# Optimization experiments

Measured on AMD Instinct MI355X. Metric: run time of the kernel, lower is better.

Reference implementation:

```python
import jax, jax.numpy as jnp
import numpy as np

# Dimensions (see shape_source): B batch, N atoms, M neighbors
B, N, M = 32, 2048, 12
F_IN, F_OUT = 64, 25          # atom_in_fea_num, atom_out_fea_num (25 fixed by Linear(25,1))
GROUPS = ((0, 683), (683, 1366), (1366, 2048))  # contiguous atom-type partition of N
EPS = 1e-5                    # BatchNorm1d eps


def setup_inputs() -> dict:
    key = jax.random.key(0)
    ks = jax.random.split(key, 9)
    atom = jax.random.normal(ks[0], (B, N, F_IN), jnp.float32)
    bond = jax.random.normal(ks[1], (B, N, M), jnp.float32)
    adj_matrix = jax.random.randint(ks[2], (B, N, M), 0, N)  # neighbor indices into N
    s_in = 1.0 / np.sqrt(F_IN)
    s_out = 1.0 / np.sqrt(F_OUT)
    # per-atom-type linear layers, stacked [G, F_IN, F_OUT]
    type_w = jax.random.uniform(ks[3], (len(GROUPS), F_IN, F_OUT), jnp.float32, -s_in, s_in)
    type_b = jax.random.uniform(ks[4], (len(GROUPS), F_OUT), jnp.float32, -s_in, s_in)
    gamma = jnp.ones((F_OUT,), jnp.float32)   # BatchNorm weight
    beta = jnp.zeros((F_OUT,), jnp.float32)   # BatchNorm bias
    conv_w = jax.random.uniform(ks[5], (F_OUT, F_OUT), jnp.float32, -s_out, s_out)
    conv_b = jax.random.uniform(ks[6], (F_OUT,), jnp.float32, -s_out, s_out)
    out_w = jax.random.uniform(ks[7], (F_OUT, 1), jnp.float32, -s_out, s_out)
    out_b = jax.random.uniform(ks[8], (1,), jnp.float32, -s_out, s_out)
    return dict(atom=atom, bond=bond, adj_matrix=adj_matrix, type_w=type_w,
                type_b=type_b, gamma=gamma, beta=beta, conv_w=conv_w,
                conv_b=conv_b, out_w=out_w, out_b=out_b)


def reference(atom, bond, adj_matrix, type_w, type_b, gamma, beta, conv_w, conv_b, out_w, out_b):
    # 1) per-atom-type grouped linear (+relu, AtomTypeLayer), scatter-assembled -> [B,N,F_OUT]
    parts = [jax.nn.relu(jnp.einsum('bnf,fo->bno', atom[:, s:e], type_w[g]) + type_b[g])
             for g, (s, e) in enumerate(GROUPS)]
    h = jnp.concatenate(parts, axis=1)
    # 2) BatchNorm1d over channels F_OUT, batch stats over (B, N); Dropout is identity in eval
    mean = h.mean(axis=(0, 1))
    var = h.var(axis=(0, 1))
    h = (h - mean) * jax.lax.rsqrt(var + EPS) * gamma + beta
    # 3) AtomConvLayer: gather neighbor features via adj_matrix, weight by bond, reduce, linear, relu
    nbr = jax.vmap(lambda hb, ab: hb[ab])(h, adj_matrix)         # [B,N,M,F_OUT]
    msg = jnp.einsum('bnm,bnmf->bnf', bond, nbr)                  # [B,N,F_OUT]
    a = jax.nn.relu(msg @ conv_w + conv_b)
    # 4) mean-pool over atoms, final linear, relu, squeeze
    e = a.mean(axis=1) @ out_w + out_b                            # [B,1]
    return jax.nn.relu(e)[..., 0]                                 # [B]
```

## Files before the change

### kernel.cpp

```cpp
#include <hip/hip_runtime.h>
#include <hip/hip_bf16.h>

#define Bn 32
#define Nn 2048
#define Mn 12
#define FIN 64
#define FOUT 25
#define HROW 32
#define EPSBN 1e-5f

#define K1_BLOCKS 1056
#define NPART K1_BLOCKS
#define K3_BLOCKS 1024
#define NROWS 65536

__global__ __launch_bounds__(256) void k1_typelinear(
    const float* __restrict__ atom,
    const float* __restrict__ type_w,
    const float* __restrict__ type_b,
    float* __restrict__ h,
    float* __restrict__ psum,
    float* __restrict__ psq)
{
    const int blk = blockIdx.x;
    const int b = blk / 33;
    const int rem = blk % 33;
    const int g = rem / 11;
    const int chunk = rem % 11;
    const int s0 = g * 683;
    const int e0 = (g == 2) ? 2048 : (g + 1) * 683;
    const int tid = threadIdx.x;
    const int a = tid & 63;
    const int q = __builtin_amdgcn_readfirstlane(tid >> 6);
    const int n = s0 + chunk * 64 + a;
    const bool act = (n < e0);

    float acc[FOUT];
    #pragma unroll
    for (int o = 0; o < FOUT; ++o) acc[o] = 0.0f;

    if (act) {
        float av[16];
        const float4* ap = reinterpret_cast<const float4*>(
            atom + ((size_t)b * Nn + n) * FIN + q * 16);
        #pragma unroll
        for (int i = 0; i < 4; ++i) {
            float4 v = ap[i];
            av[4 * i + 0] = v.x; av[4 * i + 1] = v.y;
            av[4 * i + 2] = v.z; av[4 * i + 3] = v.w;
        }
        const float* wg = type_w + (size_t)g * (FIN * FOUT) + q * 16 * FOUT;
        #pragma unroll
        for (int f = 0; f < 16; ++f) {
            const float x = av[f];
            #pragma unroll
            for (int o = 0; o < FOUT; ++o)
                acc[o] = fmaf(x, wg[f * FOUT + o], acc[o]);
        }
    }

    __shared__ float sm[3][64][26];
    if (q > 0) {
        #pragma unroll
        for (int o = 0; o < FOUT; ++o) sm[q - 1][a][o] = acc[o];
    }
    __syncthreads();
    if (q != 0) return;

    #pragma unroll
    for (int o = 0; o < FOUT; ++o)
        acc[o] += (sm[0][a][o] + sm[1][a][o]) + sm[2][a][o];

    if (act) {
        const float* bg = type_b + (size_t)g * FOUT;
        #pragma unroll
        for (int o = 0; o < FOUT; ++o)
            acc[o] = fmaxf(acc[o] + bg[o], 0.0f);
        float* hp = h + ((size_t)b * Nn + n) * HROW;
        float4* hp4 = reinterpret_cast<float4*>(hp);
        #pragma unroll
        for (int i = 0; i < 6; ++i) {
            float4 v;
            v.x = acc[4 * i + 0]; v.y = acc[4 * i + 1];
            v.z = acc[4 * i + 2]; v.w = acc[4 * i + 3];
            hp4[i] = v;
        }
        {
            float4 v; v.x = acc[24]; v.y = 0.0f; v.z = 0.0f; v.w = 0.0f;
            hp4[6] = v;
        }
    } else {
        #pragma unroll
        for (int o = 0; o < FOUT; ++o) acc[o] = 0.0f;
    }

    float bs[FOUT], bq[FOUT];
    #pragma unroll
    for (int o = 0; o < FOUT; ++o) {
        float s = acc[o];
        float qq = acc[o] * acc[o];
        #pragma unroll
        for (int m = 1; m < 64; m <<= 1) {
            s  += __shfl_xor(s,  m, 64);
            qq += __shfl_xor(qq, m, 64);
        }
        bs[o] = s; bq[o] = qq;
    }
    if (a == 0) {
        #pragma unroll
        for (int o = 0; o < FOUT; ++o)
            psum[(size_t)o * NPART + blk] = bs[o];
    } else if (a == 1) {
        #pragma unroll
        for (int o = 0; o < FOUT; ++o)
            psq[(size_t)o * NPART + blk] = bq[o];
    }
}

__global__ __launch_bounds__(256) void k2_bnstats(
    const float* __restrict__ psum,
    const float* __restrict__ psq,
    const float* __restrict__ gamma,
    const float* __restrict__ beta,
    float* __restrict__ AC)
{
    const int c = blockIdx.x;
    const int tid = threadIdx.x;
    const int lane = tid & 63;
    const int w = tid >> 6;
    const float4* ps4 = reinterpret_cast<const float4*>(psum + (size_t)c * NPART);
    const float4* pq4 = reinterpret_cast<const float4*>(psq  + (size_t)c * NPART);
    float4 v = ps4[tid];
    float4 qv = pq4[tid];
    float s1 = (v.x + v.y) + (v.z + v.w);
    float s2 = (qv.x + qv.y) + (qv.z + qv.w);
    if (tid < (NPART / 4 - 256)) {
        float4 v2 = ps4[tid + 256];
        float4 q2 = pq4[tid + 256];
        s1 += (v2.x + v2.y) + (v2.z + v2.w);
        s2 += (q2.x + q2.y) + (q2.z + q2.w);
    }
    #pragma unroll
    for (int m = 1; m < 64; m <<= 1) {
        s1 += __shfl_xor(s1, m, 64);
        s2 += __shfl_xor(s2, m, 64);
    }
    __shared__ float r1[4], r2[4];
    if (lane == 0) { r1[w] = s1; r2[w] = s2; }
    __syncthreads();
    if (tid == 0) {
        const float S1 = (r1[0] + r1[1]) + (r1[2] + r1[3]);
        const float S2 = (r2[0] + r2[1]) + (r2[2] + r2[3]);
        const float inv_cnt = 1.0f / (float)NROWS;
        const float mean = S1 * inv_cnt;
        const float var = S2 * inv_cnt - mean * mean;
        const float aa = gamma[c] * rsqrtf(var + EPSBN);
        AC[c] = aa;
        AC[28 + c] = beta[c] - mean * aa;
    }
}

__global__ __launch_bounds__(256) void k3_conv(
    const float* __restrict__ h,
    const float* __restrict__ bond,
    const int*   __restrict__ adj,
    const float* __restrict__ AC,
    const float* __restrict__ conv_w,
    const float* __restrict__ conv_b,
    const float* __restrict__ out_w,
    float* __restrict__ pe)
{
    const int blk = blockIdx.x;
    const int b = blk & 31;
    const int chunk = blk >> 5;
    const int tid = threadIdx.x;
    const int w = tid >> 6;
    const int lane = tid & 63;
    const int g = lane >> 3;
    const int c = lane & 7;

    __shared__ __align__(16) float wT[FOUT][28];
    __shared__ __align__(16) float msgn_s[4][16][36];

    for (int t = tid; t < FOUT * 28; t += 256) {
        const int o = t / 28, f = t - o * 28;
        float wv = 0.0f;
        if (f < FOUT)      wv = conv_w[f * FOUT + o];
        else if (f == 25)  wv = conv_b[o];
        else if (f == 26)  wv = out_w[o];
        wT[o][f] = wv;
    }

    const float* hb = h + (size_t)b * (Nn * HROW);
    const int atom0 = chunk * 64 + w * 16;

    const float4 Ai = *reinterpret_cast<const float4*>(AC + 4 * c);
    const float4 Ci = *reinterpret_cast<const float4*>(AC + 28 + 4 * c);

    __syncthreads();

    #pragma unroll
    for (int p = 0; p < 2; ++p) {
        const int an = atom0 + p * 8 + g;
        const size_t arow = (size_t)b * Nn + an;
        const int4*   ajp = reinterpret_cast<const int4*>(adj + arow * Mn);
        const float4* bpp = reinterpret_cast<const float4*>(bond + arow * Mn);
        const int4 A0 = ajp[0], A1 = ajp[1], A2 = ajp[2];
        const float4 B0 = bpp[0], B1 = bpp[1], B2 = bpp[2];
        const int ai[12] = {A0.x, A0.y, A0.z, A0.w,
                            A1.x, A1.y, A1.z, A1.w,
                            A2.x, A2.y, A2.z, A2.w};
        const float bw[12] = {B0.x, B0.y, B0.z, B0.w,
                              B1.x, B1.y, B1.z, B1.w,
                              B2.x, B2.y, B2.z, B2.w};
        float4 macc = {0.0f, 0.0f, 0.0f, 0.0f};
        float bsum = 0.0f;
        #pragma unroll
        for (int j = 0; j < 12; ++j) {
            const float wj = bw[j];
            bsum += wj;
            const float4 hv = *reinterpret_cast<const float4*>(
                hb + (size_t)ai[j] * HROW + c * 4);
            macc.x = fmaf(wj, hv.x, macc.x);
            macc.y = fmaf(wj, hv.y, macc.y);
            macc.z = fmaf(wj, hv.z, macc.z);
            macc.w = fmaf(wj, hv.w, macc.w);
        }
        if (c < 7) {
            float4 mn;
            mn.x = fmaf(Ai.x, macc.x, Ci.x * bsum);
            mn.y = fmaf(Ai.y, macc.y, Ci.y * bsum);
            mn.z = fmaf(Ai.z, macc.z, Ci.z * bsum);
            mn.w = fmaf(Ai.w, macc.w, Ci.w * bsum);
            if (c == 6) { mn.y = 1.0f; mn.z = 0.0f; mn.w = 0.0f; }
            *reinterpret_cast<float4*>(&msgn_s[w][p * 8 + g][4 * c]) = mn;
        }
    }

    __syncthreads();

    const int a16 = lane >> 2;
    const int mg = lane & 3;
    const float* mrow = &msgn_s[w][a16][0];
    float msv[28];
    #pragma unroll
    for (int j = 0; j < 7; ++j) {
        const float4 mv = *reinterpret_cast<const float4*>(mrow + 4 * j);
        msv[4 * j + 0] = mv.x; msv[4 * j + 1] = mv.y;
        msv[4 * j + 2] = mv.z; msv[4 * j + 3] = mv.w;
    }
    float v = 0.0f;
    #pragma unroll
    for (int k = 0; k < 7; ++k) {
        const int o = 4 * k + mg;
        if (o < FOUT) {
            const float4* wrow = reinterpret_cast<const float4*>(&wT[o][0]);
            float t = 0.0f, myow = 0.0f;
            #pragma unroll
            for (int j = 0; j < 7; ++j) {
                const float4 w4 = wrow[j];
                t = fmaf(msv[4 * j + 0], w4.x, t);
                t = fmaf(msv[4 * j + 1], w4.y, t);
                t = fmaf(msv[4 * j + 2], w4.z, t);
                t = fmaf(msv[4 * j + 3], w4.w, t);
                if (j == 6) myow = w4.z;
            }
            v += fmaxf(t, 0.0f) * myow;
        }
    }

    #pragma unroll
    for (int m = 1; m < 64; m <<= 1)
        v += __shfl_xor(v, m, 64);
    __shared__ float wsum[4];
    if (lane == 0) wsum[w] = v;
    __syncthreads();
    if (tid == 0)
        pe[blk] = (wsum[0] + wsum[1]) + (wsum[2] + wsum[3]);
}

__global__ __launch_bounds__(256) void k4_final(
    const float* __restrict__ pe,
    const float* __restrict__ out_b,
    float* __restrict__ out)
{
    const int tid = threadIdx.x;
    const float s = (pe[tid] + pe[tid + 256]) + (pe[tid + 512] + pe[tid + 768]);
    __shared__ float sred[8][33];
    sred[tid >> 5][tid & 31] = s;
    __syncthreads();
    if (tid < Bn) {
        float t = 0.0f;
        #pragma unroll
        for (int cg = 0; cg < 8; ++cg) t += sred[cg][tid];
        out[tid] = fmaxf(t * (1.0f / (float)Nn) + out_b[0], 0.0f);
    }
}

extern "C" void kernel_launch(void* const* d_in, const int* in_sizes, int n_in,
                              void* d_out, int out_size, void* d_ws, size_t ws_size,
                              hipStream_t stream)
{
    const float* atom   = (const float*)d_in[0];
    const float* bond   = (const float*)d_in[1];
    const int*   adjm   = (const int*)  d_in[2];
    const float* type_w = (const float*)d_in[3];
    const float* type_b = (const float*)d_in[4];
    const float* gamma  = (const float*)d_in[5];
    const float* beta   = (const float*)d_in[6];
    const float* conv_w = (const float*)d_in[7];
    const float* conv_b = (const float*)d_in[8];
    const float* out_w  = (const float*)d_in[9];
    const float* out_b  = (const float*)d_in[10];
    float* out = (float*)d_out;

    float* ws = (float*)d_ws;
    float* h    = ws;
    float* psum = h + (size_t)Bn * Nn * HROW;
    float* psq  = psum + (size_t)FOUT * NPART;
    float* AC   = psq + (size_t)FOUT * NPART;
    float* pe   = AC + 64;

    k1_typelinear<<<K1_BLOCKS, 256, 0, stream>>>(atom, type_w, type_b, h, psum, psq);
    k2_bnstats<<<FOUT, 256, 0, stream>>>(psum, psq, gamma, beta, AC);
    k3_conv<<<K3_BLOCKS, 256, 0, stream>>>(h, bond, adjm, AC, conv_w, conv_b, out_w, pe);
    k4_final<<<1, 256, 0, stream>>>(pe, out_b, out);
}
```

Before: 33.34 us.

## Stage atom tile and h output through LDS and spread BN stat reductions

The type-linear kernel now loads each block's 64-atom slice of `atom` into shared memory with coalesced float4 loads. It writes the `h` rows back through shared memory with coalesced stores, and the BN sum and sum-of-squares wave reductions are split across all four waves instead of only wave 0. Block indexing also puts batch in the low bits, so neighbouring blocks work on different batches. The aim is fewer uncoalesced global transactions and a shorter serial reduction tail, at the cost of an extra barrier and more LDS. Rows of the odd-stride (65-float) LDS tile are not 16-byte aligned for the float4 accesses, which may be split into narrower operations or cause alignment problems.

```diff
diff --git a/kernel.cpp b/kernel.cpp
--- a/kernel.cpp
+++ b/kernel.cpp
@@ -23,31 +23,47 @@
     float* __restrict__ psq)
 {
     const int blk = blockIdx.x;
-    const int b = blk / 33;
-    const int rem = blk % 33;
-    const int g = rem / 11;
-    const int chunk = rem % 11;
+    const int b = blk & 31;
+    const int t2 = blk >> 5;
+    const int g = t2 / 11;
+    const int chunk = t2 - g * 11;
     const int s0 = g * 683;
     const int e0 = (g == 2) ? 2048 : (g + 1) * 683;
     const int tid = threadIdx.x;
     const int a = tid & 63;
     const int q = __builtin_amdgcn_readfirstlane(tid >> 6);
-    const int n = s0 + chunk * 64 + a;
-    const bool act = (n < e0);
+    const int n0 = s0 + chunk * 64;
+
+    __shared__ __align__(16) float at[64][65];
+    __shared__ float sm[3][64][26];
+
+    {
+        const float* gbase = atom + ((size_t)b * Nn + n0) * FIN;
+        const int nrows = min(64, Nn - n0);
+        #pragma unroll
+        for (int i = 0; i < 4; ++i) {
+            const int v = tid + 256 * i;
+            const int row = v >> 4, c16 = v & 15;
+            if (row < nrows) {
+                const float4 vv = *reinterpret_cast<const float4*>(
+                    gbase + row * FIN + c16 * 4);
+                *reinterpret_cast<float4*>(&at[row][4 * c16]) = vv;
+            }
+        }
+    }
+    __syncthreads();
 
     float acc[FOUT];
     #pragma unroll
     for (int o = 0; o < FOUT; ++o) acc[o] = 0.0f;
-
-    if (act) {
+    {
         float av[16];
-        const float4* ap = reinterpret_cast<const float4*>(
-            atom + ((size_t)b * Nn + n) * FIN + q * 16);
         #pragma unroll
         for (int i = 0; i < 4; ++i) {
-            float4 v = ap[i];
-            av[4 * i + 0] = v.x; av[4 * i + 1] = v.y;
-            av[4 * i + 2] = v.z; av[4 * i + 3] = v.w;
+            const float4 vv = *reinterpret_cast<const float4*>(
+                &at[a][16 * q + 4 * i]);
+            av[4 * i + 0] = vv.x; av[4 * i + 1] = vv.y;
+            av[4 * i + 2] = vv.z; av[4 * i + 3] = vv.w;
         }
         const float* wg = type_w + (size_t)g * (FIN * FOUT) + q * 16 * FOUT;
         #pragma unroll
@@ -59,61 +75,67 @@
         }
     }
 
-    __shared__ float sm[3][64][26];
     if (q > 0) {
         #pragma unroll
         for (int o = 0; o < FOUT; ++o) sm[q - 1][a][o] = acc[o];
     }
     __syncthreads();
-    if (q != 0) return;
-
-    #pragma unroll
-    for (int o = 0; o < FOUT; ++o)
-        acc[o] += (sm[0][a][o] + sm[1][a][o]) + sm[2][a][o];
-
-    if (act) {
-        const float* bg = type_b + (size_t)g * FOUT;
+    if (q == 0) {
         #pragma unroll
         for (int o = 0; o < FOUT; ++o)
-            acc[o] = fmaxf(acc[o] + bg[o], 0.0f);
-        float* hp = h + ((size_t)b * Nn + n) * HROW;
-        float4* hp4 = reinterpret_cast<float4*>(hp);
+            acc[o] += (sm[0][a][o] + sm[1][a][o]) + sm[2][a][o];
+        const bool act = (n0 + a) < e0;
+        if (act) {
+            const float* bg = type_b + (size_t)g * FOUT;
+            #pragma unroll
+            for (int o = 0; o < FOUT; ++o)
+                acc[o] = fmaxf(acc[o] + bg[o], 0.0f);
+        } else {
+            #pragma unroll
+            for (int o = 0; o < FOUT; ++o) acc[o] = 0.0f;
+        }
         #pragma unroll
         for (int i = 0; i < 6; ++i) {
             float4 v;
             v.x = acc[4 * i + 0]; v.y = acc[4 * i + 1];
             v.z = acc[4 * i + 2]; v.w = acc[4 * i + 3];
-            hp4[i] = v;
-        }
-        {
-            float4 v; v.x = acc[24]; v.y = 0.0f; v.z = 0.0f; v.w = 0.0f;
-            hp4[6] = v;
-        }
-    } else {
-        #pragma unroll
-        for (int o = 0; o < FOUT; ++o) acc[o] = 0.0f;
-    }
-
-    float bs[FOUT], bq[FOUT];
-    #pragma unroll
-    for (int o = 0; o < FOUT; ++o) {
-        float s = acc[o];
-        float qq = acc[o] * acc[o];
-        #pragma unroll
-        for (int m = 1; m < 64; m <<= 1) {
-            s  += __shfl_xor(s,  m, 64);
-            qq += __shfl_xor(qq, m, 64);
-        }
-        bs[o] = s; bq[o] = qq;
-    }
-    if (a == 0) {
-        #pragma unroll
-        for (int o = 0; o < FOUT; ++o)
-            psum[(size_t)o * NPART + blk] = bs[o];
-    } else if (a == 1) {
-        #pragma unroll
-        for (int o = 0; o < FOUT; ++o)
-            psq[(size_t)o * NPART + blk] = bq[o];
+            *reinterpret_cast<float4*>(&at[a][4 * i]) = v;
+        }
+        at[a][24] = acc[24];
+    }
+    __syncthreads();
+
+    {
+        float* hbase = h + ((size_t)b * Nn + n0) * HROW;
+        const int nact = min(64, e0 - n0);
+        #pragma unroll
+        for (int i = 0; i < 2; ++i) {
+            const int v = tid + 256 * i;
+            const int row = v >> 3, c8 = v & 7;
+            if (row < nact) {
+                const float4 vv = *reinterpret_cast<const float4*>(
+                    &at[row][4 * c8]);
+                *reinterpret_cast<float4*>(hbase + row * HROW + 4 * c8) = vv;
+            }
+        }
+    }
+
+    const int o0 = (q == 0) ? 0 : 7 + (q - 1) * 6;
+    const int no = (q == 0) ? 7 : 6;
+    #pragma unroll
+    for (int oi = 0; oi < 7; ++oi) {
+        if (oi < no) {
+            const int o = o0 + oi;
+            const float x = at[a][o];
+            float s = x, qq = x * x;
+            #pragma unroll
+            for (int m = 1; m < 64; m <<= 1) {
+                s  += __shfl_xor(s,  m, 64);
+                qq += __shfl_xor(qq, m, 64);
+            }
+            if (a == 0) psum[(size_t)o * NPART + blk] = s;
+            else if (a == 1) psq[(size_t)o * NPART + blk] = qq;
+        }
     }
 }
 
```

Result: slower. 34.16 us (+2.5%).
